# Optimization experiments

Hardware: AMD Instinct MI355X
Metric: run time of the kernel (lower is better)

The kernel has to match this reference:

```python
import jax, jax.numpy as jnp
import numpy as np

B, T, HID, NH = 2, 2048, 1024, 16
HD = HID // NH  # head_dim = 64
ROPE_BASE = 1000000.0


def _precompute_freqs(dim, end, rope_base):
    inv = 1.0 / (rope_base ** (np.arange(0, dim, 2)[: dim // 2].astype(np.float32) / dim))
    t = np.arange(end, dtype=np.float32)
    freqs = np.outer(t, inv).astype(np.float32)  # (end, dim//2)
    cos = np.concatenate([np.cos(freqs), np.cos(freqs)], axis=-1)
    sin = np.concatenate([np.sin(freqs), np.sin(freqs)], axis=-1)
    return jnp.asarray(cos), jnp.asarray(sin)


def setup_inputs() -> dict:
    key = jax.random.key(0)
    ks = jax.random.split(key, 5)
    x = jax.random.normal(ks[0], (B, T, HID), dtype=jnp.float32)
    s = 1.0 / np.sqrt(HID)
    Wq = jax.random.normal(ks[1], (HID, HID), dtype=jnp.float32) * s
    Wk = jax.random.normal(ks[2], (HID, HID), dtype=jnp.float32) * s
    Wv = jax.random.normal(ks[3], (HID, HID), dtype=jnp.float32) * s
    Wo = jax.random.normal(ks[4], (HID, HID), dtype=jnp.float32) * s
    cos, sin = _precompute_freqs(HD, T, ROPE_BASE)
    return {"x": x, "Wq": Wq, "Wk": Wk, "Wv": Wv, "Wo": Wo, "cos": cos, "sin": sin}


def _rotate_half(u):
    half = u.shape[-1] // 2
    return jnp.concatenate([-u[..., half:], u[..., :half]], axis=-1)


def reference(x, Wq, Wk, Wv, Wo, cos, sin):
    b, t, _ = x.shape
    # projections (nn.Linear: x @ W.T)
    q = (x @ Wq.T).reshape(b, t, NH, HD).transpose(0, 2, 1, 3)  # (B,H,T,D)
    k = (x @ Wk.T).reshape(b, t, NH, HD).transpose(0, 2, 1, 3)
    v = (x @ Wv.T).reshape(b, t, NH, HD).transpose(0, 2, 1, 3)
    c = cos[None, None, :t, :]
    s = sin[None, None, :t, :]
    q = q * c + _rotate_half(q) * s
    k = k * c + _rotate_half(k) * s
    scores = jnp.einsum("bhqd,bhkd->bhqk", q, k) / jnp.sqrt(jnp.float32(HD))
    causal = jnp.tril(jnp.ones((t, t), dtype=bool))
    scores = jnp.where(causal[None, None], scores, jnp.float32(-jnp.inf))
    prob = jax.nn.softmax(scores, axis=-1)
    out = jnp.einsum("bhqk,bhkd->bhqd", prob, v)
    out = out.transpose(0, 2, 1, 3).reshape(b, t, HID)
    return out @ Wo.T
```

## Files before the change

kernel.cpp:

```cpp
#include <hip/hip_runtime.h>
#include <hip/hip_bf16.h>

#define B_   2
#define T_   2048
#define HID_ 1024
#define NH_  16
#define HD_  64
#define K_   1024
#define M_   (B_*T_)

typedef __attribute__((ext_vector_type(8)))  short bf16x8;
typedef __attribute__((ext_vector_type(4)))  float f32x4;
typedef __attribute__((ext_vector_type(16))) float f32x16;
typedef __attribute__((ext_vector_type(4)))  unsigned int u32x4;
typedef __attribute__((ext_vector_type(2)))  unsigned int u32x2;

#define LOG2E 1.44269504088896340736f

__device__ inline unsigned short f2bf(float f) {
    __hip_bfloat16 h = __float2bfloat16(f);
    return __builtin_bit_cast(unsigned short, h);
}
__device__ inline unsigned int pk2(float a, float b) {
    return (unsigned int)f2bf(a) | ((unsigned int)f2bf(b) << 16);
}
__device__ inline unsigned int pkt(float a, float b) {
    return __builtin_amdgcn_perm(__builtin_bit_cast(unsigned, a),
                                 __builtin_bit_cast(unsigned, b), 0x03020706u);
}
__device__ inline bf16x8 cvt8(float4 a, float4 b) {
    bf16x8 r;
    r[0]=(short)f2bf(a.x); r[1]=(short)f2bf(a.y); r[2]=(short)f2bf(a.z); r[3]=(short)f2bf(a.w);
    r[4]=(short)f2bf(b.x); r[5]=(short)f2bf(b.y); r[6]=(short)f2bf(b.z); r[7]=(short)f2bf(b.w);
    return r;
}

__global__ __launch_bounds__(256)
void cast_x(const float* __restrict__ in, unsigned short* __restrict__ out) {
    const int i = blockIdx.x * 256 + threadIdx.x;
    float4 a = ((const float4*)in)[2*i], b = ((const float4*)in)[2*i + 1];
    ((bf16x8*)out)[i] = cvt8(a, b);
}
__global__ __launch_bounds__(256)
void cast_w(const float* __restrict__ W0, const float* __restrict__ W1,
            const float* __restrict__ W2, const float* __restrict__ W3,
            unsigned short* __restrict__ o0, unsigned short* __restrict__ o1,
            unsigned short* __restrict__ o2, unsigned short* __restrict__ o3) {
    const int blk = blockIdx.x, sec = blk >> 9;
    const float* in = (sec == 0) ? W0 : (sec == 1) ? W1 : (sec == 2) ? W2 : W3;
    unsigned short* out = (sec == 0) ? o0 : (sec == 1) ? o1 : (sec == 2) ? o2 : o3;
    const int i = (blk & 511) * 256 + threadIdx.x;
    float4 a = ((const float4*)in)[2*i], b = ((const float4*)in)[2*i + 1];
    ((bf16x8*)out)[i] = cvt8(a, b);
}

template<int TYPE>
__global__ __launch_bounds__(256)
void gemm_k(const unsigned short* __restrict__ A, const unsigned short* __restrict__ W0,
            const unsigned short* __restrict__ W1, const unsigned short* __restrict__ W2,
            const float* __restrict__ cs, const float* __restrict__ sn,
            unsigned short* __restrict__ qb, unsigned short* __restrict__ kb,
            unsigned short* __restrict__ vtb, float* __restrict__ fout) {
    __shared__ unsigned short As[128*64];
    __shared__ unsigned short Bs[128*64];
    const int tid = threadIdx.x;
    const int w = tid >> 6, lane = tid & 63;
    const int u = lane >> 4, c = lane & 15;
    const int bm = blockIdx.x * 128, bn = blockIdx.y * 128;
    const int wm = (w & 1) * 64, wn = (w >> 1) * 64;
    const int srow = tid >> 3, scol = (tid & 7) << 3;

    const unsigned short* Wsec;
    int wrowbase;
    if constexpr (TYPE == 0) {
        const int sec = bn >> 10;
        Wsec = (sec == 0) ? W0 : ((sec == 1) ? W1 : W2);
        wrowbase = bn & 1023;
    } else {
        Wsec = W0;
        wrowbase = bn;
    }
    const unsigned short* Wp = Wsec + (size_t)(wrowbase + srow) * K_ + scol;
    const unsigned short* Ap = A + (size_t)(bm + srow) * K_ + scol;

    f32x4 acc[4][4] = {};
    bf16x8 ra[4], rb[4];

    auto loadin = [&](int k0) {
        #pragma unroll
        for (int i = 0; i < 4; ++i) {
            ra[i] = *(const bf16x8*)(Ap + (size_t)i * 32 * K_ + k0);
            rb[i] = *(const bf16x8*)(Wp + (size_t)i * 32 * K_ + k0);
        }
    };
    loadin(0);

    for (int k0 = 0; k0 < K_; k0 += 64) {
        __syncthreads();
        #pragma unroll
        for (int i = 0; i < 4; ++i) {
            const int row = i * 32 + srow;
            const int sc = (scol * 2) ^ ((row & 7) << 4);
            *(bf16x8*)((char*)As + row * 128 + sc) = ra[i];
            *(bf16x8*)((char*)Bs + row * 128 + sc) = rb[i];
        }
        __syncthreads();
        if (k0 < K_ - 64) loadin(k0 + 64);
        #pragma unroll
        for (int kk = 0; kk < 2; ++kk) {
            bf16x8 af[4], bfr[4];
            #pragma unroll
            for (int mi = 0; mi < 4; ++mi) {
                const int row = wm + mi * 16 + c;
                const int sc = (kk * 64 + u * 16) ^ ((row & 7) << 4);
                af[mi] = *(const bf16x8*)((char*)As + row * 128 + sc);
            }
            #pragma unroll
            for (int ni = 0; ni < 4; ++ni) {
                const int row = wn + ni * 16 + c;
                const int sc = (kk * 64 + u * 16) ^ ((row & 7) << 4);
                bfr[ni] = *(const bf16x8*)((char*)Bs + row * 128 + sc);
            }
            #pragma unroll
            for (int mi = 0; mi < 4; ++mi)
                #pragma unroll
                for (int ni = 0; ni < 4; ++ni)
                    acc[mi][ni] = __builtin_amdgcn_mfma_f32_16x16x32_bf16(
                        af[mi], bfr[ni], acc[mi][ni], 0, 0, 0);
        }
    }

    if constexpr (TYPE == 1) {
        #pragma unroll
        for (int mi = 0; mi < 4; ++mi)
            #pragma unroll
            for (int ni = 0; ni < 4; ++ni)
                #pragma unroll
                for (int r = 0; r < 4; ++r)
                    fout[(size_t)(bm + wm + 16*mi + 4*u + r) * HID_ + (bn + wn + 16*ni + c)] =
                        acc[mi][ni][r];
    } else {
        const int sec = bn >> 10;
        const int h = ((bn + wn) & 1023) >> 6;
        if (sec == 2) {
            #pragma unroll
            for (int mi = 0; mi < 4; ++mi)
                #pragma unroll
                for (int r = 0; r < 4; ++r) {
                    const int mg = bm + wm + 16*mi + 4*u + r;
                    const int bb = mg >> 11, t = mg & 2047;
                    #pragma unroll
                    for (int ni = 0; ni < 4; ++ni)
                        vtb[((size_t)(bb*16 + h) * 64 + 16*ni + c) * 2048 + t] =
                            f2bf(acc[mi][ni][r]);
                }
        } else {
            unsigned short* ob = sec ? kb : qb;
            const float qsc = sec ? 1.0f : (0.125f * LOG2E);
            #pragma unroll
            for (int mi = 0; mi < 4; ++mi)
                #pragma unroll
                for (int r = 0; r < 4; ++r) {
                    const int mg = bm + wm + 16*mi + 4*u + r;
                    const int bb = mg >> 11, t = mg & 2047;
                    const size_t base = ((size_t)(bb*16 + h) * 2048 + t) * 64;
                    #pragma unroll
                    for (int ni = 0; ni < 2; ++ni) {
                        const int dlo = 16*ni + c;
                        const float cv = cs[t*64 + dlo], sv = sn[t*64 + dlo];
                        const float Aa = acc[mi][ni][r], Bb = acc[mi][ni+2][r];
                        ob[base + dlo]      = f2bf((Aa*cv - Bb*sv) * qsc);
                        ob[base + dlo + 32] = f2bf((Bb*cv + Aa*sv) * qsc);
                    }
                }
        }
    }
}

__global__ __launch_bounds__(256)
void attn8(const unsigned short* __restrict__ q, const unsigned short* __restrict__ k,
           const unsigned short* __restrict__ vt, unsigned short* __restrict__ ab) {
    const int raw = blockIdx.x;
    const int bh   = (raw & 7) + 8 * ((raw >> 3) & 3);
    const int qblk = 63 - (raw >> 5);
    const int tid = threadIdx.x;
    const int wid = tid >> 6, lane = tid & 63;
    const int h = lane >> 5, c = lane & 31;
    const bool hi = (h != 0);
    const int b = bh >> 4, hh = bh & 15;
    const int q0 = qblk * 32;
    const int qgc = q0 + c;
    const unsigned short* qp = q  + (size_t)bh * (T_*64);
    const unsigned short* kp = k  + (size_t)bh * (T_*64);
    const unsigned short* vp = vt + (size_t)bh * (64*T_);

    const int kloff  = c * 64 + 8 * h;
    const int vloff0 = c * 2048 + 8 * h;
    const int vloff1 = vloff0 + 32 * 2048;

    bf16x8 qf[4];
    {
        const unsigned short* qrow = qp + (q0 + c) * 64 + 8 * h;
        #pragma unroll
        for (int s = 0; s < 4; ++s)
            qf[s] = *(const bf16x8*)(qrow + s * 16);
    }

    f32x16 O0 = {}, O1 = {};
    float m = -1e30f, lsum = 0.f;
    const int nst = qblk + 1;

    auto loadKV = [&](bf16x8 (&kf)[4], bf16x8 (&vf)[4], int st) {
        const unsigned short* kst = kp + (st << 11);
        const unsigned short* vst = vp + (st << 5);
        #pragma unroll
        for (int s = 0; s < 4; ++s)
            kf[s] = *(const bf16x8*)(kst + kloff + s * 16);
        vf[0] = *(const bf16x8*)(vst + vloff0);
        vf[1] = *(const bf16x8*)(vst + vloff0 + 16);
        vf[2] = *(const bf16x8*)(vst + vloff1);
        vf[3] = *(const bf16x8*)(vst + vloff1 + 16);
    };

    auto process = [&](const bf16x8 (&kf)[4], const bf16x8 (&vf)[4], int st) {
        const int kvs = st << 5;
        __builtin_amdgcn_s_setprio(1);
        f32x16 sa = {};
        #pragma unroll
        for (int s = 0; s < 4; ++s)
            sa = __builtin_amdgcn_mfma_f32_32x32x16_bf16(kf[s], qf[s], sa, 0, 0, 0);
        __builtin_amdgcn_s_setprio(0);
        float p[16];
        #pragma unroll
        for (int r = 0; r < 16; ++r) p[r] = sa[r];
        if (st == qblk) {
            #pragma unroll
            for (int r = 0; r < 16; ++r) {
                const int kk = kvs + (r & 3) + 8 * (r >> 2) + 4 * h;
                if (kk > qgc) p[r] = -1e30f;
            }
        }
        const float a0 = fmaxf(fmaxf(p[0],  p[1]),  p[2]);
        const float a1 = fmaxf(fmaxf(p[3],  p[4]),  p[5]);
        const float a2 = fmaxf(fmaxf(p[6],  p[7]),  p[8]);
        const float a3 = fmaxf(fmaxf(p[9],  p[10]), p[11]);
        const float a4 = fmaxf(fmaxf(p[12], p[13]), p[14]);
        float mx = fmaxf(fmaxf(fmaxf(a0, a1), fmaxf(a2, a3)), fmaxf(a4, p[15]));
        if (!__all(mx <= m + 8.0f)) {
            mx = fmaxf(mx, __shfl_xor(mx, 32));
            const float mn = fmaxf(m, mx);
            const float f = __builtin_amdgcn_exp2f(m - mn);
            m = mn;
            lsum *= f;
            #pragma unroll
            for (int r = 0; r < 16; ++r) { O0[r] *= f; O1[r] *= f; }
        }
        float ps = 0.f;
        #pragma unroll
        for (int r = 0; r < 16; ++r) {
            p[r] = __builtin_amdgcn_exp2f(p[r] - m);
            ps += p[r];
        }
        lsum += ps;
        unsigned o0 = pkt(p[0], p[1]),   o1 = pkt(p[2], p[3]);
        unsigned o2 = pkt(p[4], p[5]),   o3 = pkt(p[6], p[7]);
        unsigned o4 = pkt(p[8], p[9]),   o5 = pkt(p[10], p[11]);
        unsigned o6 = pkt(p[12], p[13]), o7 = pkt(p[14], p[15]);
        unsigned x0 = __shfl_xor(o0, 32), x1 = __shfl_xor(o1, 32);
        unsigned x2 = __shfl_xor(o2, 32), x3 = __shfl_xor(o3, 32);
        unsigned x4 = __shfl_xor(o4, 32), x5 = __shfl_xor(o5, 32);
        unsigned x6 = __shfl_xor(o6, 32), x7 = __shfl_xor(o7, 32);
        u32x4 B0w = { hi ? x2 : o0, hi ? x3 : o1, hi ? o2 : x0, hi ? o3 : x1 };
        u32x4 B1w = { hi ? x6 : o4, hi ? x7 : o5, hi ? o6 : x4, hi ? o7 : x5 };
        bf16x8 PB0 = __builtin_bit_cast(bf16x8, B0w);
        bf16x8 PB1 = __builtin_bit_cast(bf16x8, B1w);
        __builtin_amdgcn_s_setprio(1);
        O0 = __builtin_amdgcn_mfma_f32_32x32x16_bf16(vf[0], PB0, O0, 0, 0, 0);
        O0 = __builtin_amdgcn_mfma_f32_32x32x16_bf16(vf[1], PB1, O0, 0, 0, 0);
        O1 = __builtin_amdgcn_mfma_f32_32x32x16_bf16(vf[2], PB0, O1, 0, 0, 0);
        O1 = __builtin_amdgcn_mfma_f32_32x32x16_bf16(vf[3], PB1, O1, 0, 0, 0);
        __builtin_amdgcn_s_setprio(0);
    };

    bf16x8 kA[4], kB[4], vA[4], vB[4];
    if (wid < nst) loadKV(kA, vA, wid);
    for (int st = wid; st < nst; st += 8) {
        if (st + 4 < nst) loadKV(kB, vB, st + 4);
        process(kA, vA, st);
        if (st + 4 >= nst) break;
        if (st + 8 < nst) loadKV(kA, vA, st + 8);
        process(kB, vB, st + 4);
    }
    lsum += __shfl_xor(lsum, 32);

    __shared__ unsigned OSu[4][32 * 34];
    __shared__ float mS[4][32], lS[4][32];
    if (h == 0) { mS[wid][c] = m; lS[wid][c] = lsum; }
    {
        unsigned* os = &OSu[wid][0];
        const int rb = c * 34 + 2 * h;
        #pragma unroll
        for (int j = 0; j < 4; ++j) {
            os[rb + 4*j]          = pk2(O0[4*j],   O0[4*j+1]);
            os[rb + 4*j + 1]      = pk2(O0[4*j+2], O0[4*j+3]);
            os[rb + 16 + 4*j]     = pk2(O1[4*j],   O1[4*j+1]);
            os[rb + 16 + 4*j + 1] = pk2(O1[4*j+2], O1[4*j+3]);
        }
    }
    __syncthreads();

    const int ql = tid & 31, ug = (tid >> 5) * 4;
    const float M = fmaxf(fmaxf(mS[0][ql], mS[1][ql]), fmaxf(mS[2][ql], mS[3][ql]));
    float acc[8] = {};
    float L = 0.f;
    #pragma unroll
    for (int w2 = 0; w2 < 4; ++w2) {
        const float sc = __builtin_amdgcn_exp2f(mS[w2][ql] - M);
        L += lS[w2][ql] * sc;
        u32x2 pa = *(u32x2*)&OSu[w2][ql * 34 + ug];
        u32x2 pb = *(u32x2*)&OSu[w2][ql * 34 + ug + 2];
        #pragma unroll
        for (int t = 0; t < 2; ++t) {
            acc[2*t]   += __builtin_bit_cast(float, pa[t] << 16) * sc;
            acc[2*t+1] += __builtin_bit_cast(float, pa[t] & 0xffff0000u) * sc;
            acc[4+2*t]   += __builtin_bit_cast(float, pb[t] << 16) * sc;
            acc[4+2*t+1] += __builtin_bit_cast(float, pb[t] & 0xffff0000u) * sc;
        }
    }
    const float inv = 1.0f / L;
    uint4 ov;
    ov.x = pk2(acc[0]*inv, acc[1]*inv);
    ov.y = pk2(acc[2]*inv, acc[3]*inv);
    ov.z = pk2(acc[4]*inv, acc[5]*inv);
    ov.w = pk2(acc[6]*inv, acc[7]*inv);
    *(uint4*)(ab + ((size_t)(b * T_) + q0 + ql) * HID_ + hh * 64 + ug * 2) = ov;
}

extern "C" void kernel_launch(void* const* d_in, const int* in_sizes, int n_in,
                              void* d_out, int out_size, void* d_ws, size_t ws_size,
                              hipStream_t stream) {
    const float* x  = (const float*)d_in[0];
    const float* Wq = (const float*)d_in[1];
    const float* Wk = (const float*)d_in[2];
    const float* Wv = (const float*)d_in[3];
    const float* Wo = (const float*)d_in[4];
    const float* cs = (const float*)d_in[5];
    const float* sn = (const float*)d_in[6];
    char* wsb = (char*)d_ws;
    unsigned short* xb  = (unsigned short*)(wsb);
    unsigned short* wqb = (unsigned short*)(wsb + (8u  << 20));
    unsigned short* wkb = (unsigned short*)(wsb + (10u << 20));
    unsigned short* wvb = (unsigned short*)(wsb + (12u << 20));
    unsigned short* wob = (unsigned short*)(wsb + (14u << 20));
    unsigned short* qb  = (unsigned short*)(wsb + (16u << 20));
    unsigned short* kb  = (unsigned short*)(wsb + (24u << 20));
    unsigned short* vtb = (unsigned short*)(wsb + (32u << 20));
    unsigned short* ab  = (unsigned short*)(wsb + (40u << 20));

    cast_x<<<2048, 256, 0, stream>>>(x, xb);
    cast_w<<<2048, 256, 0, stream>>>(Wq, Wk, Wv, Wo, wqb, wkb, wvb, wob);

    gemm_k<0><<<dim3(M_/128, 3072/128), 256, 0, stream>>>(
        xb, wqb, wkb, wvb, cs, sn, qb, kb, vtb, nullptr);
    attn8<<<2048, 256, 0, stream>>>(qb, kb, vtb, ab);
    gemm_k<1><<<dim3(M_/128, HID_/128), 256, 0, stream>>>(
        ab, wob, nullptr, nullptr, nullptr, nullptr,
        nullptr, nullptr, nullptr, (float*)d_out);
}
```

Before: 131.2 us.

## Share K/V tiles across query-block warps and use direct global-to-LDS GEMM loads

The attention kernel now gives each block four 32-row query blocks, one per warp. The warps share double-buffered K/V tiles in LDS instead of splitting the KV range and merging partial softmax results. This removes the cross-warp combine step and cuts redundant K/V global reads, at the cost of a barrier per tile and idle warps on diagonal tiles. Separately, the GEMM now uses global_load_lds to fill LDS directly. This drops the register staging, the next-tile prefetch and the XOR swizzle, which may add bank conflicts and lose load/compute overlap.

```diff
diff --git a/kernel.cpp b/kernel.cpp
--- a/kernel.cpp
+++ b/kernel.cpp
@@ -13,7 +13,6 @@
 typedef __attribute__((ext_vector_type(4)))  float f32x4;
 typedef __attribute__((ext_vector_type(16))) float f32x16;
 typedef __attribute__((ext_vector_type(4)))  unsigned int u32x4;
-typedef __attribute__((ext_vector_type(2)))  unsigned int u32x2;
 
 #define LOG2E 1.44269504088896340736f
 
@@ -33,6 +32,11 @@
     r[0]=(short)f2bf(a.x); r[1]=(short)f2bf(a.y); r[2]=(short)f2bf(a.z); r[3]=(short)f2bf(a.w);
     r[4]=(short)f2bf(b.x); r[5]=(short)f2bf(b.y); r[6]=(short)f2bf(b.z); r[7]=(short)f2bf(b.w);
     return r;
+}
+__device__ inline void gll16(const void* g, void* l) {
+    __builtin_amdgcn_global_load_lds(
+        (const __attribute__((address_space(1))) unsigned int*)g,
+        (__attribute__((address_space(3))) unsigned int*)l, 16, 0, 0);
 }
 
 __global__ __launch_bounds__(256)
@@ -68,7 +72,6 @@
     const int u = lane >> 4, c = lane & 15;
     const int bm = blockIdx.x * 128, bn = blockIdx.y * 128;
     const int wm = (w & 1) * 64, wn = (w >> 1) * 64;
-    const int srow = tid >> 3, scol = (tid & 7) << 3;
 
     const unsigned short* Wsec;
     int wrowbase;
@@ -80,47 +83,31 @@
         Wsec = W0;
         wrowbase = bn;
     }
-    const unsigned short* Wp = Wsec + (size_t)(wrowbase + srow) * K_ + scol;
-    const unsigned short* Ap = A + (size_t)(bm + srow) * K_ + scol;
+    const unsigned short* Ab = A + (size_t)bm * K_;
+    const unsigned short* Wb = Wsec + (size_t)wrowbase * K_;
+    const int srow = lane >> 3;
+    const int scol = (lane & 7) * 8;
 
     f32x4 acc[4][4] = {};
-    bf16x8 ra[4], rb[4];
-
-    auto loadin = [&](int k0) {
-        #pragma unroll
-        for (int i = 0; i < 4; ++i) {
-            ra[i] = *(const bf16x8*)(Ap + (size_t)i * 32 * K_ + k0);
-            rb[i] = *(const bf16x8*)(Wp + (size_t)i * 32 * K_ + k0);
-        }
-    };
-    loadin(0);
 
     for (int k0 = 0; k0 < K_; k0 += 64) {
         __syncthreads();
         #pragma unroll
-        for (int i = 0; i < 4; ++i) {
-            const int row = i * 32 + srow;
-            const int sc = (scol * 2) ^ ((row & 7) << 4);
-            *(bf16x8*)((char*)As + row * 128 + sc) = ra[i];
-            *(bf16x8*)((char*)Bs + row * 128 + sc) = rb[i];
+        for (int s4 = 0; s4 < 4; ++s4) {
+            const int seg = w * 4 + s4;
+            gll16(Ab + (size_t)(seg * 8 + srow) * K_ + k0 + scol, (char*)As + seg * 1024);
+            gll16(Wb + (size_t)(seg * 8 + srow) * K_ + k0 + scol, (char*)Bs + seg * 1024);
         }
         __syncthreads();
-        if (k0 < K_ - 64) loadin(k0 + 64);
         #pragma unroll
         for (int kk = 0; kk < 2; ++kk) {
             bf16x8 af[4], bfr[4];
             #pragma unroll
-            for (int mi = 0; mi < 4; ++mi) {
-                const int row = wm + mi * 16 + c;
-                const int sc = (kk * 64 + u * 16) ^ ((row & 7) << 4);
-                af[mi] = *(const bf16x8*)((char*)As + row * 128 + sc);
-            }
-            #pragma unroll
-            for (int ni = 0; ni < 4; ++ni) {
-                const int row = wn + ni * 16 + c;
-                const int sc = (kk * 64 + u * 16) ^ ((row & 7) << 4);
-                bfr[ni] = *(const bf16x8*)((char*)Bs + row * 128 + sc);
-            }
+            for (int mi = 0; mi < 4; ++mi)
+                af[mi] = *(const bf16x8*)&As[(wm + mi*16 + c) * 64 + kk*32 + u*8];
+            #pragma unroll
+            for (int ni = 0; ni < 4; ++ni)
+                bfr[ni] = *(const bf16x8*)&Bs[(wn + ni*16 + c) * 64 + kk*32 + u*8];
             #pragma unroll
             for (int mi = 0; mi < 4; ++mi)
                 #pragma unroll
@@ -178,162 +165,145 @@
 }
 
 __global__ __launch_bounds__(256)
-void attn8(const unsigned short* __restrict__ q, const unsigned short* __restrict__ k,
+void attn9(const unsigned short* __restrict__ q, const unsigned short* __restrict__ k,
            const unsigned short* __restrict__ vt, unsigned short* __restrict__ ab) {
     const int raw = blockIdx.x;
-    const int bh   = (raw & 7) + 8 * ((raw >> 3) & 3);
-    const int qblk = 63 - (raw >> 5);
+    const int bh     = (raw & 7) + 8 * ((raw >> 3) & 3);
+    const int qchunk = 15 - (raw >> 5);
     const int tid = threadIdx.x;
     const int wid = tid >> 6, lane = tid & 63;
     const int h = lane >> 5, c = lane & 31;
     const bool hi = (h != 0);
     const int b = bh >> 4, hh = bh & 15;
-    const int q0 = qblk * 32;
-    const int qgc = q0 + c;
+    const int q0w  = qchunk * 128 + wid * 32;
+    const int qgc  = q0w + c;
+    const int NT   = qchunk * 4 + 4;
+    const int nstw = qchunk * 4 + wid + 1;
     const unsigned short* qp = q  + (size_t)bh * (T_*64);
     const unsigned short* kp = k  + (size_t)bh * (T_*64);
     const unsigned short* vp = vt + (size_t)bh * (64*T_);
 
-    const int kloff  = c * 64 + 8 * h;
-    const int vloff0 = c * 2048 + 8 * h;
-    const int vloff1 = vloff0 + 32 * 2048;
+    __shared__ unsigned short Kls[2][32*72];
+    __shared__ unsigned short Vls[2][64*40];
+
+    const int skr = tid >> 3, skc = (tid & 7) * 8;
+    const int svd = tid >> 2, svc = (tid & 3) * 8;
+    const unsigned short* kg = kp + skr * 64 + skc;
+    const unsigned short* vg = vp + (size_t)svd * 2048 + svc;
 
     bf16x8 qf[4];
     {
-        const unsigned short* qrow = qp + (q0 + c) * 64 + 8 * h;
+        const unsigned short* qrow = qp + (q0w + c) * 64 + 8 * h;
         #pragma unroll
-        for (int s = 0; s < 4; ++s)
-            qf[s] = *(const bf16x8*)(qrow + s * 16);
+        for (int s = 0; s < 4; ++s) qf[s] = *(const bf16x8*)(qrow + s * 16);
     }
 
     f32x16 O0 = {}, O1 = {};
     float m = -1e30f, lsum = 0.f;
-    const int nst = qblk + 1;
-
-    auto loadKV = [&](bf16x8 (&kf)[4], bf16x8 (&vf)[4], int st) {
-        const unsigned short* kst = kp + (st << 11);
-        const unsigned short* vst = vp + (st << 5);
-        #pragma unroll
-        for (int s = 0; s < 4; ++s)
-            kf[s] = *(const bf16x8*)(kst + kloff + s * 16);
-        vf[0] = *(const bf16x8*)(vst + vloff0);
-        vf[1] = *(const bf16x8*)(vst + vloff0 + 16);
-        vf[2] = *(const bf16x8*)(vst + vloff1);
-        vf[3] = *(const bf16x8*)(vst + vloff1 + 16);
-    };
-
-    auto process = [&](const bf16x8 (&kf)[4], const bf16x8 (&vf)[4], int st) {
-        const int kvs = st << 5;
-        __builtin_amdgcn_s_setprio(1);
-        f32x16 sa = {};
-        #pragma unroll
-        for (int s = 0; s < 4; ++s)
-            sa = __builtin_amdgcn_mfma_f32_32x32x16_bf16(kf[s], qf[s], sa, 0, 0, 0);
-        __builtin_amdgcn_s_setprio(0);
-        float p[16];
-        #pragma unroll
-        for (int r = 0; r < 16; ++r) p[r] = sa[r];
-        if (st == qblk) {
+
+    {
+        uint4 kr = *(const uint4*)kg;
+        uint4 vr = *(const uint4*)vg;
+        *(uint4*)&Kls[0][skr * 72 + skc] = kr;
+        *(uint4*)&Vls[0][svd * 40 + svc] = vr;
+    }
+    __syncthreads();
+
+    for (int st = 0; st < NT; ++st) {
+        const int bi = st & 1;
+        const bool more = (st + 1 < NT);
+        uint4 kr, vr;
+        if (more) {
+            kr = *(const uint4*)(kg + (size_t)(st + 1) * 2048);
+            vr = *(const uint4*)(vg + (st + 1) * 32);
+        }
+        if (st < nstw) {
+            bf16x8 kf[4], vf[4];
+            #pragma unroll
+            for (int s = 0; s < 4; ++s)
+                kf[s] = *(const bf16x8*)&Kls[bi][c * 72 + s * 16 + 8 * h];
+            #pragma unroll
+            for (int s = 0; s < 4; ++s)
+                vf[s] = *(const bf16x8*)&Vls[bi][(((s >> 1) << 5) + c) * 40
+                                                 + ((s & 1) << 4) + 8 * h];
+            const int kvs = st << 5;
+            __builtin_amdgcn_s_setprio(1);
+            f32x16 sa = {};
+            #pragma unroll
+            for (int s = 0; s < 4; ++s)
+                sa = __builtin_amdgcn_mfma_f32_32x32x16_bf16(kf[s], qf[s], sa, 0, 0, 0);
+            __builtin_amdgcn_s_setprio(0);
+            float p[16];
+            #pragma unroll
+            for (int r = 0; r < 16; ++r) p[r] = sa[r];
+            if (st == nstw - 1) {
+                #pragma unroll
+                for (int r = 0; r < 16; ++r) {
+                    const int kk = kvs + (r & 3) + 8 * (r >> 2) + 4 * h;
+                    if (kk > qgc) p[r] = -1e30f;
+                }
+            }
+            const float a0 = fmaxf(fmaxf(p[0],  p[1]),  p[2]);
+            const float a1 = fmaxf(fmaxf(p[3],  p[4]),  p[5]);
+            const float a2 = fmaxf(fmaxf(p[6],  p[7]),  p[8]);
+            const float a3 = fmaxf(fmaxf(p[9],  p[10]), p[11]);
+            const float a4 = fmaxf(fmaxf(p[12], p[13]), p[14]);
+            float mx = fmaxf(fmaxf(fmaxf(a0, a1), fmaxf(a2, a3)), fmaxf(a4, p[15]));
+            if (!__all(mx <= m + 8.0f)) {
+                mx = fmaxf(mx, __shfl_xor(mx, 32));
+                const float mn = fmaxf(m, mx);
+                const float f = __builtin_amdgcn_exp2f(m - mn);
+                m = mn;
+                lsum *= f;
+                #pragma unroll
+                for (int r = 0; r < 16; ++r) { O0[r] *= f; O1[r] *= f; }
+            }
+            float ps = 0.f;
             #pragma unroll
             for (int r = 0; r < 16; ++r) {
-                const int kk = kvs + (r & 3) + 8 * (r >> 2) + 4 * h;
-                if (kk > qgc) p[r] = -1e30f;
+                p[r] = __builtin_amdgcn_exp2f(p[r] - m);
+                ps += p[r];
             }
-        }
-        const float a0 = fmaxf(fmaxf(p[0],  p[1]),  p[2]);
-        const float a1 = fmaxf(fmaxf(p[3],  p[4]),  p[5]);
-        const float a2 = fmaxf(fmaxf(p[6],  p[7]),  p[8]);
-        const float a3 = fmaxf(fmaxf(p[9],  p[10]), p[11]);
-        const float a4 = fmaxf(fmaxf(p[12], p[13]), p[14]);
-        float mx = fmaxf(fmaxf(fmaxf(a0, a1), fmaxf(a2, a3)), fmaxf(a4, p[15]));
-        if (!__all(mx <= m + 8.0f)) {
-            mx = fmaxf(mx, __shfl_xor(mx, 32));
-            const float mn = fmaxf(m, mx);
-            const float f = __builtin_amdgcn_exp2f(m - mn);
-            m = mn;
-            lsum *= f;
-            #pragma unroll
-            for (int r = 0; r < 16; ++r) { O0[r] *= f; O1[r] *= f; }
-        }
-        float ps = 0.f;
-        #pragma unroll
-        for (int r = 0; r < 16; ++r) {
-            p[r] = __builtin_amdgcn_exp2f(p[r] - m);
-            ps += p[r];
-        }
-        lsum += ps;
-        unsigned o0 = pkt(p[0], p[1]),   o1 = pkt(p[2], p[3]);
-        unsigned o2 = pkt(p[4], p[5]),   o3 = pkt(p[6], p[7]);
-        unsigned o4 = pkt(p[8], p[9]),   o5 = pkt(p[10], p[11]);
-        unsigned o6 = pkt(p[12], p[13]), o7 = pkt(p[14], p[15]);
-        unsigned x0 = __shfl_xor(o0, 32), x1 = __shfl_xor(o1, 32);
-        unsigned x2 = __shfl_xor(o2, 32), x3 = __shfl_xor(o3, 32);
-        unsigned x4 = __shfl_xor(o4, 32), x5 = __shfl_xor(o5, 32);
-        unsigned x6 = __shfl_xor(o6, 32), x7 = __shfl_xor(o7, 32);
-        u32x4 B0w = { hi ? x2 : o0, hi ? x3 : o1, hi ? o2 : x0, hi ? o3 : x1 };
-        u32x4 B1w = { hi ? x6 : o4, hi ? x7 : o5, hi ? o6 : x4, hi ? o7 : x5 };
-        bf16x8 PB0 = __builtin_bit_cast(bf16x8, B0w);
-        bf16x8 PB1 = __builtin_bit_cast(bf16x8, B1w);
-        __builtin_amdgcn_s_setprio(1);
-        O0 = __builtin_amdgcn_mfma_f32_32x32x16_bf16(vf[0], PB0, O0, 0, 0, 0);
-        O0 = __builtin_amdgcn_mfma_f32_32x32x16_bf16(vf[1], PB1, O0, 0, 0, 0);
-        O1 = __builtin_amdgcn_mfma_f32_32x32x16_bf16(vf[2], PB0, O1, 0, 0, 0);
-        O1 = __builtin_amdgcn_mfma_f32_32x32x16_bf16(vf[3], PB1, O1, 0, 0, 0);
-        __builtin_amdgcn_s_setprio(0);
-    };
-
-    bf16x8 kA[4], kB[4], vA[4], vB[4];
-    if (wid < nst) loadKV(kA, vA, wid);
-    for (int st = wid; st < nst; st += 8) {
-        if (st + 4 < nst) loadKV(kB, vB, st + 4);
-        process(kA, vA, st);
-        if (st + 4 >= nst) break;
-        if (st + 8 < nst) loadKV(kA, vA, st + 8);
-        process(kB, vB, st + 4);
-    }
+            lsum += ps;
+            unsigned o0 = pkt(p[0], p[1]),   o1 = pkt(p[2], p[3]);
+            unsigned o2 = pkt(p[4], p[5]),   o3 = pkt(p[6], p[7]);
+            unsigned o4 = pkt(p[8], p[9]),   o5 = pkt(p[10], p[11]);
+            unsigned o6 = pkt(p[12], p[13]), o7 = pkt(p[14], p[15]);
+            unsigned x0 = __shfl_xor(o0, 32), x1 = __shfl_xor(o1, 32);
+            unsigned x2 = __shfl_xor(o2, 32), x3 = __shfl_xor(o3, 32);
+            unsigned x4 = __shfl_xor(o4, 32), x5 = __shfl_xor(o5, 32);
+            unsigned x6 = __shfl_xor(o6, 32), x7 = __shfl_xor(o7, 32);
+            u32x4 B0w = { hi ? x2 : o0, hi ? x3 : o1, hi ? o2 : x0, hi ? o3 : x1 };
+            u32x4 B1w = { hi ? x6 : o4, hi ? x7 : o5, hi ? o6 : x4, hi ? o7 : x5 };
+            bf16x8 PB0 = __builtin_bit_cast(bf16x8, B0w);
+            bf16x8 PB1 = __builtin_bit_cast(bf16x8, B1w);
+            __builtin_amdgcn_s_setprio(1);
+            O0 = __builtin_amdgcn_mfma_f32_32x32x16_bf16(vf[0], PB0, O0, 0, 0, 0);
+            O0 = __builtin_amdgcn_mfma_f32_32x32x16_bf16(vf[1], PB1, O0, 0, 0, 0);
+            O1 = __builtin_amdgcn_mfma_f32_32x32x16_bf16(vf[2], PB0, O1, 0, 0, 0);
+            O1 = __builtin_amdgcn_mfma_f32_32x32x16_bf16(vf[3], PB1, O1, 0, 0, 0);
+            __builtin_amdgcn_s_setprio(0);
+        }
+        if (more) {
+            *(uint4*)&Kls[bi ^ 1][skr * 72 + skc] = kr;
+            *(uint4*)&Vls[bi ^ 1][svd * 40 + svc] = vr;
+        }
+        __syncthreads();
+    }
+
     lsum += __shfl_xor(lsum, 32);
-
-    __shared__ unsigned OSu[4][32 * 34];
-    __shared__ float mS[4][32], lS[4][32];
-    if (h == 0) { mS[wid][c] = m; lS[wid][c] = lsum; }
-    {
-        unsigned* os = &OSu[wid][0];
-        const int rb = c * 34 + 2 * h;
-        #pragma unroll
-        for (int j = 0; j < 4; ++j) {
-            os[rb + 4*j]          = pk2(O0[4*j],   O0[4*j+1]);
-            os[rb + 4*j + 1]      = pk2(O0[4*j+2], O0[4*j+3]);
-            os[rb + 16 + 4*j]     = pk2(O1[4*j],   O1[4*j+1]);
-            os[rb + 16 + 4*j + 1] = pk2(O1[4*j+2], O1[4*j+3]);
-        }
-    }
-    __syncthreads();
-
-    const int ql = tid & 31, ug = (tid >> 5) * 4;
-    const float M = fmaxf(fmaxf(mS[0][ql], mS[1][ql]), fmaxf(mS[2][ql], mS[3][ql]));
-    float acc[8] = {};
-    float L = 0.f;
+    const float inv = 1.0f / lsum;
+    unsigned short* orow = ab + ((size_t)(b * T_) + q0w + c) * HID_ + hh * 64;
     #pragma unroll
-    for (int w2 = 0; w2 < 4; ++w2) {
-        const float sc = __builtin_amdgcn_exp2f(mS[w2][ql] - M);
-        L += lS[w2][ql] * sc;
-        u32x2 pa = *(u32x2*)&OSu[w2][ql * 34 + ug];
-        u32x2 pb = *(u32x2*)&OSu[w2][ql * 34 + ug + 2];
-        #pragma unroll
-        for (int t = 0; t < 2; ++t) {
-            acc[2*t]   += __builtin_bit_cast(float, pa[t] << 16) * sc;
-            acc[2*t+1] += __builtin_bit_cast(float, pa[t] & 0xffff0000u) * sc;
-            acc[4+2*t]   += __builtin_bit_cast(float, pb[t] << 16) * sc;
-            acc[4+2*t+1] += __builtin_bit_cast(float, pb[t] & 0xffff0000u) * sc;
-        }
-    }
-    const float inv = 1.0f / L;
-    uint4 ov;
-    ov.x = pk2(acc[0]*inv, acc[1]*inv);
-    ov.y = pk2(acc[2]*inv, acc[3]*inv);
-    ov.z = pk2(acc[4]*inv, acc[5]*inv);
-    ov.w = pk2(acc[6]*inv, acc[7]*inv);
-    *(uint4*)(ab + ((size_t)(b * T_) + q0 + ql) * HID_ + hh * 64 + ug * 2) = ov;
+    for (int j = 0; j < 4; ++j) {
+        uint2 v0, v1;
+        v0.x = pk2(O0[4*j] * inv,   O0[4*j+1] * inv);
+        v0.y = pk2(O0[4*j+2] * inv, O0[4*j+3] * inv);
+        v1.x = pk2(O1[4*j] * inv,   O1[4*j+1] * inv);
+        v1.y = pk2(O1[4*j+2] * inv, O1[4*j+3] * inv);
+        *(uint2*)(orow + 8*j + 4*h)      = v0;
+        *(uint2*)(orow + 32 + 8*j + 4*h) = v1;
+    }
 }
 
 extern "C" void kernel_launch(void* const* d_in, const int* in_sizes, int n_in,
@@ -362,7 +332,7 @@
 
     gemm_k<0><<<dim3(M_/128, 3072/128), 256, 0, stream>>>(
         xb, wqb, wkb, wvb, cs, sn, qb, kb, vtb, nullptr);
-    attn8<<<2048, 256, 0, stream>>>(qb, kb, vtb, ab);
+    attn9<<<512, 256, 0, stream>>>(qb, kb, vtb, ab);
     gemm_k<1><<<dim3(M_/128, HID_/128), 256, 0, stream>>>(
         ab, wob, nullptr, nullptr, nullptr, nullptr,
         nullptr, nullptr, nullptr, (float*)d_out);
```

Result: slower. 160.1 us (+22.0%).
